# Kernel optimization log

Measured on AMD Instinct MI355X. Metric: run time of the kernel, lower is better.

## Reference

```python
import jax, jax.numpy as jnp
import numpy as np

FEAT_DIMS = [119, 9, 11, 12, 9, 5, 8, 2, 2]
EDGE_DIMS = [22, 6, 2]           # actual edge feature cardinalities
EDGE_TAB_DIMS = [119, 9, 11]     # table sizes (source code reuses feat_dims for edges)
H = 512
HE = 128
OUT = 1024
L = 6
B = 1024        # graphs
NPG = 32        # nodes per graph
N = B * NPG     # 32768 nodes
E = N * 4       # 131072 edges
EPG = E // B    # edges per graph
EPS = 1e-5
NODE_OFF = np.concatenate([[0], np.cumsum(FEAT_DIMS)[:-1]]).astype(np.int32)
EDGE_OFF = np.concatenate([[0], np.cumsum(EDGE_TAB_DIMS)[:-1]]).astype(np.int32)


def setup_inputs():
    key = jax.random.key(0)
    ks = iter(jax.random.split(key, 64))
    nk = lambda: next(ks)
    x = jnp.stack([jax.random.randint(nk(), (N,), 0, d) for d in FEAT_DIMS], axis=1)
    edge_attr = jnp.stack([jax.random.randint(nk(), (E,), 0, d) for d in EDGE_DIMS], axis=1)
    eg = jnp.arange(E) // EPG  # graph id per edge; endpoints stay inside the graph
    src = eg * NPG + jax.random.randint(nk(), (E,), 0, NPG)
    dst = eg * NPG + jax.random.randint(nk(), (E,), 0, NPG)
    edge_index = jnp.stack([src, dst], axis=0)
    batch = jnp.arange(N) // NPG
    w = lambda *s: jax.random.normal(nk(), s, jnp.float32) * 0.02
    return dict(
        x=x, edge_attr=edge_attr, edge_index=edge_index, batch=batch,
        node_tab=w(sum(FEAT_DIMS), H),
        edge_tab=w(sum(EDGE_TAB_DIMS), HE),
        bondW=w(L, HE, H), bondB=jnp.zeros((L, H)),
        bondG=jnp.ones((L, H)), bondBeta=jnp.zeros((L, H)),
        atomW1=w(L, H, 2 * H), atomB1=jnp.zeros((L, 2 * H)),
        atomG=jnp.ones((L, 2 * H)), atomBeta=jnp.zeros((L, 2 * H)),
        atomW2=w(L, 2 * H, H), atomB2=jnp.zeros((L, H)),
        normG=jnp.ones((L, H)), normB=jnp.zeros((L, H)),
        outW=w(H, OUT), outB=jnp.zeros((OUT,)),
        gapW=w(OUT, H), gapB=jnp.zeros((H,)),
        attW=w(H, 1), attB=jnp.zeros((1,)),
        projW=w(OUT, OUT), projB=jnp.zeros((OUT,)),
    )


def _bn(v, g, b):
    # training-mode BatchNorm1d over the row (node/edge) dimension
    m = v.mean(0)
    var = ((v - m) ** 2).mean(0)
    return (v - m) * jax.lax.rsqrt(var + EPS) * g + b


def reference(x, edge_attr, edge_index, batch, node_tab, edge_tab, bondW, bondB, bondG, bondBeta, atomW1, atomB1, atomG, atomBeta, atomW2, atomB2, normG, normB, outW, outB, gapW, gapB, attW, attB, projW, projB):
    # AtomEncoder: sum of per-column embedding lookups via offset-concatenated tables
    z = node_tab[x + jnp.asarray(NODE_OFF)].sum(1)              # [N, H]
    e_emb = edge_tab[edge_attr + jnp.asarray(EDGE_OFF)].sum(1)  # [E, HE]
    src, dst = edge_index[0], edge_index[1]

    def layer(z, p):
        bW, bB, bG, bBe, aW1, aB1, aG, aBe, aW2, aB2, nG, nB = p
        ee = jax.nn.relu(_bn(e_emb @ bW + bB, bG, bBe))         # mlp_bond: [E, H]
        msg = z[src] + ee                                       # gather + add (message)
        agg = jax.ops.segment_sum(msg, dst, num_segments=N)     # scatter-add aggregate
        h = jax.nn.relu(_bn((z + agg) @ aW1 + aB1, aG, aBe))    # mlp_atom layer 1
        z = h @ aW2 + aB2                                       # mlp_atom layer 2
        z = jax.nn.relu(_bn(z, nG, nB))                         # outer BN + ReLU; dropout = identity (eval)
        return z, None

    z, _ = jax.lax.scan(layer, z, (bondW, bondB, bondG, bondBeta, atomW1, atomB1, atomG, atomBeta, atomW2, atomB2, normG, normB))
    z = z @ outW + outB                                         # [N, OUT]

    # to_dense_batch (batch is sorted; NPG nodes per graph)
    counts = jax.ops.segment_sum(jnp.ones((N,), jnp.int32), batch, num_segments=B)
    starts = jnp.cumsum(counts) - counts
    pos = jnp.arange(N) - starts[batch]
    dense = jnp.zeros((B, NPG, OUT), z.dtype).at[batch, pos].set(z)   # [B, NPG, OUT]
    mask = jnp.zeros((B, NPG), z.dtype).at[batch, pos].set(1.0)       # [B, NPG]

    zg = dense @ gapW + gapB                                    # [B, NPG, H]
    att = zg @ attW + attB                                      # [B, NPG, 1]
    alpha = jax.nn.softmax(att, axis=1)
    h_graph = jnp.sum(dense * alpha * mask[..., None], axis=1)  # [B, OUT]
    return h_graph @ projW + projB                              # [B, OUT]
```

## Files before the change

### kernel.cpp

```cpp
#include <hip/hip_runtime.h>
#include <hip/hip_bf16.h>
#include <stdint.h>

using bf16 = __hip_bfloat16;
typedef __attribute__((ext_vector_type(8))) short short8;
typedef __attribute__((ext_vector_type(4))) float floatx4;

#define N_NODES  32768
#define N_EDGES  131072
#define N_GRAPH  1024
#define NPG      32
#define EPG      128
#define H_DIM    512
#define HE_DIM   128
#define OUT_DIM  1024
#define N_LAYERS 6
#define MC_ROWS  8192

__device__ __forceinline__ float b2f(bf16 v) { return __bfloat162float(v); }
__device__ __forceinline__ bf16  f2b(float f) { return __float2bfloat16(f); }
__device__ __forceinline__ floatx4 mfma16(short8 a, short8 b, floatx4 c) {
    return __builtin_amdgcn_mfma_f32_16x16x32_bf16(a, b, c, 0, 0, 0);
}
__device__ __forceinline__ float ldf(const void* p, size_t i, int isf) {
    return isf ? ((const float*)p)[i] : b2f(((const bf16*)p)[i]);
}
__device__ __forceinline__ void gload_lds16(const void* g, void* l) {
    __builtin_amdgcn_global_load_lds(
        (const __attribute__((address_space(1))) unsigned int*)g,
        (__attribute__((address_space(3))) unsigned int*)l, 16, 0, 0);
}

__device__ const int NODE_OFFS[9] = {0,119,128,139,151,160,165,173,175};

__global__ __launch_bounds__(256)
void k_detect(const unsigned short* __restrict__ tab, int n, int* __restrict__ flag)
{
    int big = 0;
    for (int i = threadIdx.x; i < n; i += 256) {
        unsigned short u = tab[i];
        int e = (u >> 7) & 0xFF;
        if (e >= 0x88) big++;
    }
    __shared__ int r[256];
    r[threadIdx.x] = big;
    __syncthreads();
    for (int s = 128; s > 0; s >>= 1) {
        if (threadIdx.x < s) r[threadIdx.x] += r[threadIdx.x + s];
        __syncthreads();
    }
    if (threadIdx.x == 0) *flag = (r[0] > 64) ? 1 : 0;
}

__global__ __launch_bounds__(64)
void k_edge_sort(const int* __restrict__ edge_index, short* __restrict__ sortedE,
                 int* __restrict__ estarts)
{
    const int g = blockIdx.x, t = threadIdx.x;
    __shared__ int d[128];
    __shared__ int off[33];
    d[t]      = edge_index[N_EDGES + g * EPG + t]      - g * NPG;
    d[t + 64] = edge_index[N_EDGES + g * EPG + t + 64] - g * NPG;
    __syncthreads();
    if (t < 32) {
        int c = 0;
        for (int e = 0; e < 128; ++e) c += (d[e] == t) ? 1 : 0;
        off[t + 1] = c;
    }
    __syncthreads();
    if (t == 0) {
        off[0] = 0;
        for (int n = 1; n <= 32; ++n) off[n] += off[n - 1];
    }
    __syncthreads();
    if (t < 33) estarts[g * 33 + t] = off[t];
    if (t < 32) {
        int p = off[t];
        for (int e = 0; e < 128; ++e)
            if (d[e] == t) sortedE[g * EPG + p++] = (short)e;
    }
}

__global__ __launch_bounds__(256)
void k_transpose(const void* __restrict__ W, size_t woff, bf16* __restrict__ Wt,
                 int K, int N, const int* __restrict__ flagp)
{
    const int isf = *flagp;
    __shared__ bf16 tile[64][72];
    const int nb = blockIdx.x * 64, kb = blockIdx.y * 64;
    const int t = threadIdx.x;
    const int r = t >> 2, c0 = (t & 3) * 16;
    if (isf) {
        const float* src = (const float*)W + woff + (size_t)(kb + r) * N + nb + c0;
#pragma unroll
        for (int i = 0; i < 16; ++i) tile[r][c0 + i] = f2b(src[i]);
    } else {
        const bf16* src = (const bf16*)W + woff + (size_t)(kb + r) * N + nb + c0;
        *(uint4*)&tile[r][c0]     = ((const uint4*)src)[0];
        *(uint4*)&tile[r][c0 + 8] = ((const uint4*)src)[1];
    }
    __syncthreads();
    __align__(16) bf16 vals[16];
#pragma unroll
    for (int i = 0; i < 16; ++i) vals[i] = tile[c0 + i][r];
    bf16* dst = Wt + (size_t)(nb + r) * K + kb + c0;
    *(uint4*)dst       = *(uint4*)&vals[0];
    *(uint4*)(dst + 8) = *(uint4*)&vals[8];
}

__global__ __launch_bounds__(512)
void k_node_embed(const int* __restrict__ x, const void* __restrict__ tab,
                  float* __restrict__ Z, const int* __restrict__ flagp)
{
    const int isf = *flagp;
    const int n = blockIdx.x, t = threadIdx.x;
    __shared__ int xi[9];
    if (t < 9) xi[t] = NODE_OFFS[t] + x[(size_t)n * 9 + t];
    __syncthreads();
    float s = 0.f;
#pragma unroll
    for (int f = 0; f < 9; ++f) s += ldf(tab, (size_t)xi[f] * H_DIM + t, isf);
    Z[(size_t)n * H_DIM + t] = s;
}

__global__ __launch_bounds__(256)
void k_bond_gram(const int* __restrict__ ea, const void* __restrict__ etab,
                 float* __restrict__ S, float* __restrict__ mu, const int* __restrict__ flagp)
{
    const int isf = *flagp;
    const int tid = threadIdx.x;
    const int lane = tid & 63, wv = tid >> 6, q = lane >> 4, l15 = lane & 15;
    __shared__ __align__(16) bf16 Et[128][136];
    __shared__ int eix[128][3];

    floatx4 acc[2][8];
#pragma unroll
    for (int i = 0; i < 2; ++i)
#pragma unroll
        for (int j = 0; j < 8; ++j) acc[i][j] = (floatx4){0.f,0.f,0.f,0.f};
    float muacc = 0.f;
    const int e0 = blockIdx.x * 512;

    for (int r = 0; r < 4; ++r) {
        __syncthreads();
        if (tid < 128) {
            int e = e0 + r * 128 + tid;
            eix[tid][0] = ea[(size_t)e * 3 + 0];
            eix[tid][1] = 119 + ea[(size_t)e * 3 + 1];
            eix[tid][2] = 128 + ea[(size_t)e * 3 + 2];
        }
        __syncthreads();
        {
            int c = tid & 127, eh = (tid >> 7) * 64;
            for (int e = eh; e < eh + 64; e += 2) {
                float s0 = ldf(etab, (size_t)eix[e][0] * HE_DIM + c, isf)
                         + ldf(etab, (size_t)eix[e][1] * HE_DIM + c, isf)
                         + ldf(etab, (size_t)eix[e][2] * HE_DIM + c, isf);
                float s1 = ldf(etab, (size_t)eix[e+1][0] * HE_DIM + c, isf)
                         + ldf(etab, (size_t)eix[e+1][1] * HE_DIM + c, isf)
                         + ldf(etab, (size_t)eix[e+1][2] * HE_DIM + c, isf);
                bf16 h0 = f2b(s0), h1 = f2b(s1);
                unsigned int pk = (unsigned int)*(unsigned short*)&h0
                                | ((unsigned int)*(unsigned short*)&h1 << 16);
                *(unsigned int*)&Et[c][e] = pk;
                muacc += b2f(h0) + b2f(h1);
            }
        }
        __syncthreads();
#pragma unroll
        for (int kc = 0; kc < 4; ++kc) {
            short8 a0 = *(const short8*)&Et[wv * 32 + l15][kc * 32 + q * 8];
            short8 a1 = *(const short8*)&Et[wv * 32 + 16 + l15][kc * 32 + q * 8];
#pragma unroll
            for (int nt = 0; nt < 8; ++nt) {
                short8 b = *(const short8*)&Et[nt * 16 + l15][kc * 32 + q * 8];
                acc[0][nt] = mfma16(a0, b, acc[0][nt]);
                acc[1][nt] = mfma16(a1, b, acc[1][nt]);
            }
        }
    }
#pragma unroll
    for (int mt = 0; mt < 2; ++mt)
#pragma unroll
        for (int nt = 0; nt < 8; ++nt)
#pragma unroll
            for (int rr = 0; rr < 4; ++rr) {
                int row = wv * 32 + mt * 16 + q * 4 + rr;
                atomicAdd(&S[(size_t)row * 128 + nt * 16 + l15], acc[mt][nt][rr]);
            }
    atomicAdd(&mu[tid & 127], muacc);
}

__global__ __launch_bounds__(128)
void k_bond_fold(const float* __restrict__ S, const float* __restrict__ mu,
                 const bf16* __restrict__ bWt,
                 const void* __restrict__ bG, const void* __restrict__ bBe, size_t go,
                 float* __restrict__ scale1, float* __restrict__ shift1,
                 const int* __restrict__ flagp)
{
    const int isf = *flagp;
    const int j = blockIdx.x;
    const int k = threadIdx.x;
    __shared__ float wbuf[128];
    __shared__ float rp[2][2];
    wbuf[k] = b2f(bWt[(size_t)j * 128 + k]);
    __syncthreads();
    float wk = wbuf[k];
    float dot = 0.f;
    for (int m = 0; m < 128; ++m) dot += S[(size_t)m * 128 + k] * wbuf[m];
    float p1 = wk * dot;
    float p2 = mu[k] * wk;
    for (int off = 32; off > 0; off >>= 1) {
        p1 += __shfl_down(p1, off, 64);
        p2 += __shfl_down(p2, off, 64);
    }
    if ((k & 63) == 0) { rp[k >> 6][0] = p1; rp[k >> 6][1] = p2; }
    __syncthreads();
    if (k == 0) {
        const float invE = 1.f / (float)N_EDGES;
        float mean = (rp[0][1] + rp[1][1]) * invE;
        float var  = (rp[0][0] + rp[1][0]) * invE - mean * mean;
        var = var < 0.f ? 0.f : var;
        float rstd = rsqrtf(var + 1e-5f);
        float sc = ldf(bG, go + j, isf) * rstd;
        scale1[j] = sc;
        shift1[j] = ldf(bBe, go + j, isf) - mean * sc;
    }
}

__global__ __launch_bounds__(256)
void k_bond_gemm_agg(const int* __restrict__ ea, const void* __restrict__ etab,
                     const bf16* __restrict__ bWt,
                     const int* __restrict__ edge_index,
                     const short* __restrict__ sortedE, const int* __restrict__ estarts,
                     const float* __restrict__ Z,
                     const float* __restrict__ scale1, const float* __restrict__ shift1,
                     const float* __restrict__ zsc, const float* __restrict__ zsh,
                     float* __restrict__ X2, const int* __restrict__ flagp)
{
    const int isf = *flagp;
    const int tid = threadIdx.x;
    const int lane = tid & 63, wv = tid >> 6, q = lane >> 4, l15 = lane & 15;
    const int nc = blockIdx.x;
    const int g  = blockIdx.y;

    __shared__ __align__(16) char smem[54784];
    bf16 (*As)[136] = (bf16(*)[136])smem;
    bf16 (*Bs)[136] = (bf16(*)[136])(smem + 34816);
    float (*Cs)[68] = (float(*)[68])smem;
    int*   srcl = (int*)(smem + 52224);
    short* sid  = (short*)(smem + 52736);
    int*   sst  = (int*)(smem + 52992);
    int (*eix)[3] = (int(*)[3])(smem + 53248);

    if (tid < 128) {
        int e = g * EPG + tid;
        srcl[tid] = edge_index[e];
        sid[tid]  = sortedE[g * EPG + tid];
        eix[tid][0] = ea[(size_t)e * 3 + 0];
        eix[tid][1] = 119 + ea[(size_t)e * 3 + 1];
        eix[tid][2] = 128 + ea[(size_t)e * 3 + 2];
    }
    if (tid >= 128 && tid < 161) sst[tid - 128] = estarts[g * 33 + (tid - 128)];
    __syncthreads();
    {
        int row = tid >> 1, half = (tid & 1) * 64;
        int eb[3] = {eix[row][0], eix[row][1], eix[row][2]};
#pragma unroll
        for (int seg = 0; seg < 4; ++seg) {
            float a16[16];
#pragma unroll
            for (int j = 0; j < 16; ++j) a16[j] = 0.f;
#pragma unroll
            for (int f = 0; f < 3; ++f) {
                size_t base = (size_t)eb[f] * HE_DIM + half + seg * 16;
                if (isf) {
                    const float4* s = (const float4*)((const float*)etab + base);
#pragma unroll
                    for (int v = 0; v < 4; ++v) {
                        float4 t = s[v];
                        a16[v*4+0] += t.x; a16[v*4+1] += t.y;
                        a16[v*4+2] += t.z; a16[v*4+3] += t.w;
                    }
                } else {
                    const bf16* s = (const bf16*)etab + base;
#pragma unroll
                    for (int j = 0; j < 16; ++j) a16[j] += b2f(s[j]);
                }
            }
#pragma unroll
            for (int j = 0; j < 16; ++j) As[row][half + seg * 16 + j] = f2b(a16[j]);
        }
    }
    {
        int row = tid >> 2, seg = (tid & 3) * 32;
        const bf16* src = bWt + (size_t)(nc * 64 + row) * 128 + seg;
        uint4 v0 = ((const uint4*)src)[0];
        uint4 v1 = ((const uint4*)src)[1];
        uint4 v2 = ((const uint4*)src)[2];
        uint4 v3 = ((const uint4*)src)[3];
        *(uint4*)(&Bs[row][seg +  0]) = v0;
        *(uint4*)(&Bs[row][seg +  8]) = v1;
        *(uint4*)(&Bs[row][seg + 16]) = v2;
        *(uint4*)(&Bs[row][seg + 24]) = v3;
    }
    __syncthreads();

    floatx4 acc[2][4];
#pragma unroll
    for (int i = 0; i < 2; ++i)
#pragma unroll
        for (int jj = 0; jj < 4; ++jj) acc[i][jj] = (floatx4){0.f,0.f,0.f,0.f};
    const int m0 = wv * 32;
#pragma unroll
    for (int kk = 0; kk < 4; ++kk) {
        int k0 = kk * 32;
        short8 a0 = *(const short8*)(&As[m0 + l15][k0 + q * 8]);
        short8 a1 = *(const short8*)(&As[m0 + 16 + l15][k0 + q * 8]);
#pragma unroll
        for (int nt = 0; nt < 4; ++nt) {
            short8 bfr = *(const short8*)(&Bs[nt * 16 + l15][k0 + q * 8]);
            acc[0][nt] = mfma16(a0, bfr, acc[0][nt]);
            acc[1][nt] = mfma16(a1, bfr, acc[1][nt]);
        }
    }
    __syncthreads();
#pragma unroll
    for (int mt = 0; mt < 2; ++mt)
#pragma unroll
        for (int nt = 0; nt < 4; ++nt)
#pragma unroll
            for (int r = 0; r < 4; ++r)
                Cs[m0 + mt * 16 + q * 4 + r][nt * 16 + l15] = acc[mt][nt][r];
    __syncthreads();
    {
        int j = tid & 63, eg = (tid >> 6) * 32;
        int col = nc * 64 + j;
        float sc = scale1[col], sh = shift1[col];
        float zs = zsc ? zsc[col] : 1.f, zh = zsc ? zsh[col] : 0.f;
#pragma unroll 4
        for (int e = eg; e < eg + 32; ++e) {
            float y = Cs[e][j] * sc + sh;
            y = y > 0.f ? y : 0.f;
            float zv = Z[(size_t)srcl[e] * H_DIM + col];
            if (zsc) { zv = zv * zs + zh; zv = zv > 0.f ? zv : 0.f; }
            Cs[e][j] = y + zv;
        }
    }
    __syncthreads();
    {
        int j = tid & 63, base = (tid >> 6) * 8;
        int col = nc * 64 + j;
        float zs = zsc ? zsc[col] : 1.f, zh = zsc ? zsh[col] : 0.f;
#pragma unroll
        for (int r = 0; r < 8; ++r) {
            int n = base + r;
            int s0 = sst[n], s1 = sst[n + 1];
            float a = 0.f;
            for (int idx = s0; idx < s1; ++idx)
                a += Cs[sid[idx]][j];
            size_t zi = (size_t)(g * NPG + n) * H_DIM + col;
            float zv = Z[zi];
            if (zsc) { zv = zv * zs + zh; zv = zv > 0.f ? zv : 0.f; }
            X2[zi] = a + zv;
        }
    }
}

__global__ __launch_bounds__(256, 2)
void k_gemm(const void* __restrict__ Av, int aMode,
            const float* __restrict__ bnsc, const float* __restrict__ bnsh,
            const bf16* __restrict__ Bt,
            void* __restrict__ Cv, int cMode,
            const void* __restrict__ bias, const int* __restrict__ flagp,
            int statsMode, float* __restrict__ cs, float* __restrict__ cq,
            int K, int lda, int ldc, int mStoreMin)
{
    const int tid  = threadIdx.x;
    const int lane = tid & 63;
    const int wv   = tid >> 6;
    const int q    = lane >> 4;
    const int l15  = lane & 15;
    const int wm   = wv & 1;
    const int wn   = wv >> 1;
    const int m0   = blockIdx.y * 128;
    const int n0   = blockIdx.x * 128;

    __shared__ __align__(16) bf16 As[128][40];
    __shared__ __align__(16) bf16 Bs[128][32];

    floatx4 acc[4][4];
#pragma unroll
    for (int mt = 0; mt < 4; ++mt)
#pragma unroll
        for (int nt = 0; nt < 4; ++nt) acc[mt][nt] = (floatx4){0.f,0.f,0.f,0.f};

    const int ar = tid >> 1;
    const int ak = (tid & 1) * 16;
    const bf16* BtBase = Bt + (size_t)n0 * K;
    const int cb0 = wv * 64;
    const int cb1 = (4 + wv) * 64;

    for (int k0 = 0; k0 < K; k0 += 32) {
        short av[16];
        if (aMode == 1) {
            const float* Ap = (const float*)Av + (size_t)(m0 + ar) * lda + k0 + ak;
#pragma unroll
            for (int i = 0; i < 16; i += 4) {
                float4 f = *(const float4*)(Ap + i);
                bf16 h0 = f2b(f.x), h1 = f2b(f.y), h2 = f2b(f.z), h3 = f2b(f.w);
                av[i] = *(short*)&h0; av[i+1] = *(short*)&h1;
                av[i+2] = *(short*)&h2; av[i+3] = *(short*)&h3;
            }
        } else {
            const bf16* Ap = (const bf16*)Av + (size_t)(m0 + ar) * lda + k0 + ak;
            *(uint4*)&av[0] = *(const uint4*)Ap;
            *(uint4*)&av[8] = *(const uint4*)(Ap + 8);
            if (aMode == 2) {
#pragma unroll
                for (int i = 0; i < 16; ++i) {
                    bf16 h = *(bf16*)&av[i];
                    float f = b2f(h) * bnsc[k0 + ak + i] + bnsh[k0 + ak + i];
                    f = f > 0.f ? f : 0.f;
                    bf16 o = f2b(f);
                    av[i] = *(short*)&o;
                }
            }
        }
        __syncthreads();
        {
            int c0i = cb0 + lane;
            gload_lds16(BtBase + (size_t)(c0i >> 2) * K + k0 + (c0i & 3) * 8,
                        &Bs[0][0] + (size_t)cb0 * 8);
            int c1i = cb1 + lane;
            gload_lds16(BtBase + (size_t)(c1i >> 2) * K + k0 + (c1i & 3) * 8,
                        &Bs[0][0] + (size_t)cb1 * 8);
        }
        *(uint4*)(&As[ar][ak])     = *(uint4*)&av[0];
        *(uint4*)(&As[ar][ak + 8]) = *(uint4*)&av[8];
        __syncthreads();
        short8 af[4], bfr[4];
#pragma unroll
        for (int mt = 0; mt < 4; ++mt)
            af[mt] = *(const short8*)(&As[wm * 64 + mt * 16 + l15][q * 8]);
#pragma unroll
        for (int nt = 0; nt < 4; ++nt)
            bfr[nt] = *(const short8*)(&Bs[wn * 64 + nt * 16 + l15][q * 8]);
#pragma unroll
        for (int mt = 0; mt < 4; ++mt)
#pragma unroll
            for (int nt = 0; nt < 4; ++nt)
                acc[mt][nt] = mfma16(af[mt], bfr[nt], acc[mt][nt]);
    }

    const int isf = flagp ? *flagp : 0;
    int cm = cMode;
    if (cMode == 3) cm = isf ? 2 : 1;
    float bvv[4] = {0.f, 0.f, 0.f, 0.f};
    if (bias) {
#pragma unroll
        for (int nt = 0; nt < 4; ++nt)
            bvv[nt] = ldf(bias, (size_t)n0 + wn * 64 + nt * 16 + l15, isf);
    }
    if (cm) {
#pragma unroll
        for (int mt = 0; mt < 4; ++mt)
#pragma unroll
            for (int r = 0; r < 4; ++r) {
                int row = m0 + wm * 64 + mt * 16 + q * 4 + r;
                if (row < mStoreMin) continue;
                size_t crow = (size_t)(row - mStoreMin) * ldc + n0;
                if (cm == 2) {
                    float* Crow = (float*)Cv + crow;
#pragma unroll
                    for (int nt = 0; nt < 4; ++nt)
                        Crow[wn * 64 + nt * 16 + l15] = acc[mt][nt][r] + bvv[nt];
                } else {
                    bf16* Crow = (bf16*)Cv + crow;
#pragma unroll
                    for (int nt = 0; nt < 4; ++nt)
                        Crow[wn * 64 + nt * 16 + l15] = f2b(acc[mt][nt][r] + bvv[nt]);
                }
            }
    }
    if (statsMode) {
        float ls[4], lq[4];
#pragma unroll
        for (int nt = 0; nt < 4; ++nt) { ls[nt] = 0.f; lq[nt] = 0.f; }
#pragma unroll
        for (int nt = 0; nt < 4; ++nt)
#pragma unroll
            for (int mt = 0; mt < 4; ++mt)
#pragma unroll
                for (int r = 0; r < 4; ++r) {
                    float v = acc[mt][nt][r];
                    if (statsMode == 1) v = b2f(f2b(v));
                    ls[nt] += v; lq[nt] += v * v;
                }
        float* red = (float*)&As[0][0];
        __syncthreads();
        red[tid] = 0.f;
        __syncthreads();
#pragma unroll
        for (int nt = 0; nt < 4; ++nt) {
            int col = wn * 64 + nt * 16 + l15;
            atomicAdd(&red[col * 2],     ls[nt]);
            atomicAdd(&red[col * 2 + 1], lq[nt]);
        }
        __syncthreads();
        if (tid < 128) {
            atomicAdd(&cs[n0 + tid], red[tid * 2]);
            atomicAdd(&cq[n0 + tid], red[tid * 2 + 1]);
        }
    }
}

__global__ __launch_bounds__(256)
void k_bn_finalize(const float* __restrict__ cs, const float* __restrict__ cq,
                   const void* __restrict__ g, const void* __restrict__ be, size_t goff,
                   int cols, float invR, float* __restrict__ scale, float* __restrict__ shift,
                   const int* __restrict__ flagp)
{
    const int isf = *flagp;
    int c = blockIdx.x * 256 + threadIdx.x;
    if (c < cols) {
        float mean = cs[c] * invR;
        float var = cq[c] * invR - mean * mean;
        var = var < 0.f ? 0.f : var;
        float rstd = rsqrtf(var + 1e-5f);
        float sc = ldf(g, goff + c, isf) * rstd;
        scale[c] = sc;
        shift[c] = ldf(be, goff + c, isf) - mean * sc;
    }
}

__global__ __launch_bounds__(256)
void k_bn_apply_relu_f32(float* __restrict__ X, const float* __restrict__ scale,
                         const float* __restrict__ shift, int colmask, unsigned int nvec4)
{
    unsigned int i = blockIdx.x * 256 + threadIdx.x;
    if (i >= nvec4) return;
    float4* p = (float4*)X + i;
    int cbase = (int)(((size_t)i * 4) & (size_t)colmask);
    float4 v = *p;
    float f;
    f = v.x * scale[cbase+0] + shift[cbase+0]; v.x = f > 0.f ? f : 0.f;
    f = v.y * scale[cbase+1] + shift[cbase+1]; v.y = f > 0.f ? f : 0.f;
    f = v.z * scale[cbase+2] + shift[cbase+2]; v.z = f > 0.f ? f : 0.f;
    f = v.w * scale[cbase+3] + shift[cbase+3]; v.w = f > 0.f ? f : 0.f;
    *p = v;
}

__global__ __launch_bounds__(256)
void k_att_v(const void* __restrict__ gapW, const void* __restrict__ gapB,
             const void* __restrict__ attW, const void* __restrict__ attB,
             float* __restrict__ v, const int* __restrict__ flagp)
{
    const int isf = *flagp;
    const int lane = threadIdx.x & 63, wv = threadIdx.x >> 6;
    if (blockIdx.x == 256) {
        if (wv == 0) {
            float s = 0.f;
            for (int k = lane; k < 512; k += 64) s += ldf(gapB, k, isf) * ldf(attW, k, isf);
            for (int off = 32; off > 0; off >>= 1) s += __shfl_down(s, off, 64);
            if (lane == 0) v[1024] = s + ldf(attB, 0, isf);
        }
        return;
    }
    const int o = blockIdx.x * 4 + wv;
    float s = 0.f;
    for (int k = lane; k < 512; k += 64) s += ldf(gapW, (size_t)o * 512 + k, isf) * ldf(attW, k, isf);
    for (int off = 32; off > 0; off >>= 1) s += __shfl_down(s, off, 64);
    if (lane == 0) v[o] = s;
}

__global__ __launch_bounds__(256)
void k_qv(const void* __restrict__ outW, const void* __restrict__ outB,
          const float* __restrict__ v, float* __restrict__ qv, const int* __restrict__ flagp)
{
    const int isf = *flagp;
    const int lane = threadIdx.x & 63, wv = threadIdx.x >> 6;
    if (blockIdx.x == 128) {
        if (wv == 0) {
            float s = 0.f;
            for (int o = lane; o < 1024; o += 64) s += ldf(outB, o, isf) * v[o];
            for (int off = 32; off > 0; off >>= 1) s += __shfl_down(s, off, 64);
            if (lane == 0) qv[512] = s + v[1024];
        }
        return;
    }
    const int k = blockIdx.x * 4 + wv;
    float s = 0.f;
    for (int o = lane; o < 1024; o += 64) s += ldf(outW, (size_t)k * 1024 + o, isf) * v[o];
    for (int off = 32; off > 0; off >>= 1) s += __shfl_down(s, off, 64);
    if (lane == 0) qv[k] = s;
}

__global__ __launch_bounds__(256)
void k_att_dot(const float* __restrict__ Z, const float* __restrict__ qv, float* __restrict__ att)
{
    const int lane = threadIdx.x & 63, wv = threadIdx.x >> 6;
    const int row = blockIdx.x * 4 + wv;
    const float* p = Z + (size_t)row * 512 + lane * 8;
    float s = 0.f;
#pragma unroll
    for (int i = 0; i < 8; ++i) s += p[i] * qv[lane * 8 + i];
    for (int off = 32; off > 0; off >>= 1) s += __shfl_down(s, off, 64);
    if (lane == 0) att[row] = s + qv[512];
}

__global__ __launch_bounds__(256)
void k_softmax_pool(const float* __restrict__ Z, const float* __restrict__ att, bf16* __restrict__ ZG)
{
    const int g = blockIdx.x, t = threadIdx.x;
    __shared__ float alpha[32];
    if (t < 32) alpha[t] = att[g * 32 + t];
    __syncthreads();
    if (t == 0) {
        float mx = alpha[0];
        for (int p = 1; p < 32; ++p) mx = fmaxf(mx, alpha[p]);
        float sum = 0.f;
        for (int p = 0; p < 32; ++p) { float e = __expf(alpha[p] - mx); alpha[p] = e; sum += e; }
        float inv = 1.f / sum;
        for (int p = 0; p < 32; ++p) alpha[p] *= inv;
    }
    __syncthreads();
#pragma unroll
    for (int ci = 0; ci < 2; ++ci) {
        int c = t + ci * 256;
        float acc = 0.f;
        for (int p = 0; p < 32; ++p)
            acc += alpha[p] * Z[(size_t)(g * 32 + p) * 512 + c];
        ZG[(size_t)g * 512 + c] = f2b(acc);
    }
}

extern "C" void kernel_launch(void* const* d_in, const int* in_sizes, int n_in,
                              void* d_out, int out_size, void* d_ws, size_t ws_size,
                              hipStream_t stream)
{
    (void)in_sizes; (void)n_in; (void)out_size; (void)ws_size;
    const int*  x          = (const int*)d_in[0];
    const int*  edge_attr  = (const int*)d_in[1];
    const int*  edge_index = (const int*)d_in[2];
    const void* node_tab   = d_in[4];
    const void* edge_tab   = d_in[5];
    const void* bondW      = d_in[6];
    const void* bondG      = d_in[8];
    const void* bondBeta   = d_in[9];
    const void* atomW1     = d_in[10];
    const void* atomG      = d_in[12];
    const void* atomBeta   = d_in[13];
    const void* atomW2     = d_in[14];
    const void* normG      = d_in[16];
    const void* normB      = d_in[17];
    const void* outW       = d_in[18];
    const void* outB       = d_in[19];
    const void* gapW       = d_in[20];
    const void* gapB       = d_in[21];
    const void* attW       = d_in[22];
    const void* attB       = d_in[23];
    const void* projW      = d_in[24];
    const void* projB      = d_in[25];

    char* ws = (char*)d_ws;
    float* z      = (float*)ws;
    bf16*  Uc     = (bf16*)(ws + 67108864ull);
    bf16*  zg     = Uc;
    bf16*  hg     = (bf16*)(ws + 67108864ull + 1048576ull);
    bf16*  projWt = (bf16*)(ws + 67108864ull + 4194304ull);
    bf16*  W1t    = (bf16*)(ws + 83886080ull);
    bf16*  W2t    = (bf16*)(ws + 84934656ull);
    bf16*  bWt    = (bf16*)(ws + 85983232ull);
    bf16*  outWt  = W1t;
    char*  st  = ws + 86114304ull;
    int*   flag = (int*)(st);
    float* S    = (float*)(st + 256);
    float* mu   = (float*)(st + 65792);
    float* cs   = (float*)(st + 66304);
    float* cq   = (float*)(st + 70400);
    float* cs2  = (float*)(st + 74496);
    float* cq2  = (float*)(st + 76544);
    float* sc1  = (float*)(st + 78592);
    float* sh1  = (float*)(st + 82688);
    float* sc2  = (float*)(st + 86784);
    float* sh2  = (float*)(st + 88832);
    float* vv   = (float*)(st + 90880);
    float* qv   = (float*)(st + 95232);
    float* att  = (float*)(st + 97536);
    short* sortedE = (short*)(st + 228608);
    int*   estarts = (int*)(st + 490752);

    k_detect<<<1, 256, 0, stream>>>((const unsigned short*)node_tab, 4096, flag);
    k_edge_sort<<<N_GRAPH, 64, 0, stream>>>(edge_index, sortedE, estarts);
    hipMemsetAsync(st + 256, 0, 66048, stream);
    k_bond_gram<<<256, 256, 0, stream>>>(edge_attr, edge_tab, S, mu, flag);
    k_node_embed<<<N_NODES, 512, 0, stream>>>(x, node_tab, z, flag);

    for (int l = 0; l < N_LAYERS; ++l) {
        const float* zscp = (l == 0) ? nullptr : sc2;
        const float* zshp = (l == 0) ? nullptr : sh2;

        k_transpose<<<dim3(16, 8), 256, 0, stream>>>(atomW1, (size_t)l * 512 * 1024, W1t, 512, 1024, flag);
        k_transpose<<<dim3(8, 16), 256, 0, stream>>>(atomW2, (size_t)l * 1024 * 512, W2t, 1024, 512, flag);
        k_transpose<<<dim3(8, 2), 256, 0, stream>>>(bondW, (size_t)l * 128 * 512, bWt, 128, 512, flag);

        k_bond_fold<<<512, 128, 0, stream>>>(S, mu, bWt, bondG, bondBeta, (size_t)l * 512, sc1, sh1, flag);
        k_bond_gemm_agg<<<dim3(8, N_GRAPH), 256, 0, stream>>>(edge_attr, edge_tab, bWt,
                                                              edge_index, sortedE, estarts,
                                                              z, sc1, sh1, zscp, zshp, z, flag);

        hipMemsetAsync(cs, 0, 12288, stream);
        k_gemm<<<dim3(8, 256), 256, 0, stream>>>(z, 1, nullptr, nullptr, W1t,
                                                 Uc, 1, nullptr, nullptr,
                                                 1, cs, cq, 512, 512, 1024, 24576);
        k_bn_finalize<<<4, 256, 0, stream>>>(cs, cq, atomG, atomBeta, (size_t)l * 1024,
                                             1024, 1.f / 32768.f, sc1, sh1, flag);
        for (int mi = 0; mi < 4; ++mi) {
            int mc = (mi + 3) & 3;
            float* zc = z + (size_t)mc * MC_ROWS * 512;
            if (mc != 3)
                k_gemm<<<dim3(8, 64), 256, 0, stream>>>(zc, 1, nullptr, nullptr, W1t,
                                                        Uc, 1, nullptr, nullptr,
                                                        0, nullptr, nullptr, 512, 512, 1024, 0);
            k_gemm<<<dim3(4, 64), 256, 0, stream>>>(Uc, 2, sc1, sh1, W2t,
                                                    zc, 2, nullptr, nullptr,
                                                    2, cs2, cq2, 1024, 1024, 512, 0);
        }
        k_bn_finalize<<<2, 256, 0, stream>>>(cs2, cq2, normG, normB, (size_t)l * 512,
                                             512, 1.f / 32768.f, sc2, sh2, flag);
    }
    k_bn_apply_relu_f32<<<16384, 256, 0, stream>>>(z, sc2, sh2, 511, 4194304u);

    k_att_v<<<257, 256, 0, stream>>>(gapW, gapB, attW, attB, vv, flag);
    k_qv<<<129, 256, 0, stream>>>(outW, outB, vv, qv, flag);
    k_att_dot<<<8192, 256, 0, stream>>>(z, qv, att);
    k_softmax_pool<<<N_GRAPH, 256, 0, stream>>>(z, att, zg);
    k_transpose<<<dim3(16, 8), 256, 0, stream>>>(outW, 0, outWt, 512, 1024, flag);
    k_gemm<<<dim3(8, 8), 256, 0, stream>>>(zg, 0, nullptr, nullptr, outWt,
                                           hg, 1, outB, flag,
                                           0, nullptr, nullptr, 512, 512, 1024, 0);
    k_transpose<<<dim3(16, 16), 256, 0, stream>>>(projW, 0, projWt, 1024, 1024, flag);
    k_gemm<<<dim3(8, 8), 256, 0, stream>>>(hg, 0, nullptr, nullptr, projWt,
                                           d_out, 3, projB, flag,
                                           0, nullptr, nullptr, 1024, 1024, 1024, 0);
}
```

Before: 4.425 ms.

## Precompute bf16 edge embeddings once and scatter GEMM outputs into destination-sorted order

Adds a one-time kernel that sums the three edge-table rows per edge into a bf16 buffer in workspace, so each layer's bond kernel (8 column-blocks × 6 layers) loads those rows directly instead of redoing three table gathers. The bond kernel also writes its accumulators into shared memory at each edge's sorted rank, so the per-node aggregation reads contiguous rows rather than doing indirect lookups. The cost is a 32 MB workspace buffer, used only when the workspace is large enough, plus one extra launch.

```diff
diff --git a/kernel.cpp b/kernel.cpp
--- a/kernel.cpp
+++ b/kernel.cpp
@@ -79,6 +79,22 @@
         for (int e = 0; e < 128; ++e)
             if (d[e] == t) sortedE[g * EPG + p++] = (short)e;
     }
+}
+
+__global__ __launch_bounds__(512)
+void k_edge_embed(const int* __restrict__ ea, const void* __restrict__ etab,
+                  bf16* __restrict__ Ebf, const int* __restrict__ flagp)
+{
+    const int isf = *flagp;
+    const int t = threadIdx.x;
+    const int sub = t >> 7, c = t & 127;
+    const int e = blockIdx.x * 4 + sub;
+    size_t eb = (size_t)e * 3;
+    int i0 = ea[eb], i1 = 119 + ea[eb + 1], i2 = 128 + ea[eb + 2];
+    float s = ldf(etab, (size_t)i0 * HE_DIM + c, isf);
+    s += ldf(etab, (size_t)i1 * HE_DIM + c, isf);
+    s += ldf(etab, (size_t)i2 * HE_DIM + c, isf);
+    Ebf[(size_t)e * HE_DIM + c] = f2b(s);
 }
 
 __global__ __launch_bounds__(256)
@@ -230,6 +246,7 @@
 
 __global__ __launch_bounds__(256)
 void k_bond_gemm_agg(const int* __restrict__ ea, const void* __restrict__ etab,
+                     const bf16* __restrict__ Ebf,
                      const bf16* __restrict__ bWt,
                      const int* __restrict__ edge_index,
                      const short* __restrict__ sortedE, const int* __restrict__ estarts,
@@ -244,52 +261,62 @@
     const int nc = blockIdx.x;
     const int g  = blockIdx.y;
 
-    __shared__ __align__(16) char smem[54784];
+    __shared__ __align__(16) char smem[53136];
     bf16 (*As)[136] = (bf16(*)[136])smem;
     bf16 (*Bs)[136] = (bf16(*)[136])(smem + 34816);
     float (*Cs)[68] = (float(*)[68])smem;
-    int*   srcl = (int*)(smem + 52224);
-    short* sid  = (short*)(smem + 52736);
-    int*   sst  = (int*)(smem + 52992);
-    int (*eix)[3] = (int(*)[3])(smem + 53248);
+    int*   srcs = (int*)(smem + 52224);
+    int*   sst  = (int*)(smem + 52736);
+    short* rank = (short*)(smem + 52872);
 
     if (tid < 128) {
-        int e = g * EPG + tid;
-        srcl[tid] = edge_index[e];
-        sid[tid]  = sortedE[g * EPG + tid];
-        eix[tid][0] = ea[(size_t)e * 3 + 0];
-        eix[tid][1] = 119 + ea[(size_t)e * 3 + 1];
-        eix[tid][2] = 128 + ea[(size_t)e * 3 + 2];
+        int p = tid;
+        int e = (int)sortedE[g * EPG + p];
+        rank[e] = (short)p;
+        srcs[p] = edge_index[g * EPG + e];
     }
     if (tid >= 128 && tid < 161) sst[tid - 128] = estarts[g * 33 + (tid - 128)];
-    __syncthreads();
+
     {
         int row = tid >> 1, half = (tid & 1) * 64;
-        int eb[3] = {eix[row][0], eix[row][1], eix[row][2]};
-#pragma unroll
-        for (int seg = 0; seg < 4; ++seg) {
-            float a16[16];
-#pragma unroll
-            for (int j = 0; j < 16; ++j) a16[j] = 0.f;
-#pragma unroll
-            for (int f = 0; f < 3; ++f) {
-                size_t base = (size_t)eb[f] * HE_DIM + half + seg * 16;
-                if (isf) {
-                    const float4* s = (const float4*)((const float*)etab + base);
-#pragma unroll
-                    for (int v = 0; v < 4; ++v) {
-                        float4 t = s[v];
-                        a16[v*4+0] += t.x; a16[v*4+1] += t.y;
-                        a16[v*4+2] += t.z; a16[v*4+3] += t.w;
+        if (Ebf) {
+            const uint4* src = (const uint4*)(Ebf + (size_t)(g * EPG + row) * HE_DIM + half);
+            uint4 v[8];
+#pragma unroll
+            for (int i = 0; i < 8; ++i) v[i] = src[i];
+#pragma unroll
+            for (int i = 0; i < 8; ++i) *(uint4*)(&As[row][half + 8 * i]) = v[i];
+        } else {
+            size_t eb = (size_t)(g * EPG + row) * 3;
+            int ebi[3];
+            ebi[0] = ea[eb];
+            ebi[1] = 119 + ea[eb + 1];
+            ebi[2] = 128 + ea[eb + 2];
+#pragma unroll
+            for (int seg = 0; seg < 4; ++seg) {
+                float a16[16];
+#pragma unroll
+                for (int j = 0; j < 16; ++j) a16[j] = 0.f;
+#pragma unroll
+                for (int f = 0; f < 3; ++f) {
+                    size_t base = (size_t)ebi[f] * HE_DIM + half + seg * 16;
+                    if (isf) {
+                        const float4* s = (const float4*)((const float*)etab + base);
+#pragma unroll
+                        for (int v = 0; v < 4; ++v) {
+                            float4 t = s[v];
+                            a16[v*4+0] += t.x; a16[v*4+1] += t.y;
+                            a16[v*4+2] += t.z; a16[v*4+3] += t.w;
+                        }
+                    } else {
+                        const bf16* s = (const bf16*)etab + base;
+#pragma unroll
+                        for (int j = 0; j < 16; ++j) a16[j] += b2f(s[j]);
                     }
-                } else {
-                    const bf16* s = (const bf16*)etab + base;
-#pragma unroll
-                    for (int j = 0; j < 16; ++j) a16[j] += b2f(s[j]);
                 }
+#pragma unroll
+                for (int j = 0; j < 16; ++j) As[row][half + seg * 16 + j] = f2b(a16[j]);
             }
-#pragma unroll
-            for (int j = 0; j < 16; ++j) As[row][half + seg * 16 + j] = f2b(a16[j]);
         }
     }
     {
@@ -325,26 +352,31 @@
         }
     }
     __syncthreads();
-#pragma unroll
-    for (int mt = 0; mt < 2; ++mt)
-#pragma unroll
-        for (int nt = 0; nt < 4; ++nt)
-#pragma unroll
-            for (int r = 0; r < 4; ++r)
-                Cs[m0 + mt * 16 + q * 4 + r][nt * 16 + l15] = acc[mt][nt][r];
-    __syncthreads();
     {
-        int j = tid & 63, eg = (tid >> 6) * 32;
+#pragma unroll
+        for (int mt = 0; mt < 2; ++mt)
+#pragma unroll
+            for (int r = 0; r < 4; ++r) {
+                int row = m0 + mt * 16 + q * 4 + r;
+                int rp = (int)rank[row];
+#pragma unroll
+                for (int nt = 0; nt < 4; ++nt)
+                    Cs[rp][nt * 16 + l15] = acc[mt][nt][r];
+            }
+    }
+    __syncthreads();
+    {
+        int j = tid & 63, pg = (tid >> 6) * 32;
         int col = nc * 64 + j;
         float sc = scale1[col], sh = shift1[col];
         float zs = zsc ? zsc[col] : 1.f, zh = zsc ? zsh[col] : 0.f;
 #pragma unroll 4
-        for (int e = eg; e < eg + 32; ++e) {
-            float y = Cs[e][j] * sc + sh;
+        for (int p = pg; p < pg + 32; ++p) {
+            float y = Cs[p][j] * sc + sh;
             y = y > 0.f ? y : 0.f;
-            float zv = Z[(size_t)srcl[e] * H_DIM + col];
+            float zv = Z[(size_t)srcs[p] * H_DIM + col];
             if (zsc) { zv = zv * zs + zh; zv = zv > 0.f ? zv : 0.f; }
-            Cs[e][j] = y + zv;
+            Cs[p][j] = y + zv;
         }
     }
     __syncthreads();
@@ -358,7 +390,7 @@
             int s0 = sst[n], s1 = sst[n + 1];
             float a = 0.f;
             for (int idx = s0; idx < s1; ++idx)
-                a += Cs[sid[idx]][j];
+                a += Cs[idx][j];
             size_t zi = (size_t)(g * NPG + n) * H_DIM + col;
             float zv = Z[zi];
             if (zsc) { zv = zv * zs + zh; zv = zv > 0.f ? zv : 0.f; }
@@ -639,7 +671,7 @@
                               void* d_out, int out_size, void* d_ws, size_t ws_size,
                               hipStream_t stream)
 {
-    (void)in_sizes; (void)n_in; (void)out_size; (void)ws_size;
+    (void)in_sizes; (void)n_in; (void)out_size;
     const int*  x          = (const int*)d_in[0];
     const int*  edge_attr  = (const int*)d_in[1];
     const int*  edge_index = (const int*)d_in[2];
@@ -690,12 +722,15 @@
     float* att  = (float*)(st + 97536);
     short* sortedE = (short*)(st + 228608);
     int*   estarts = (int*)(st + 490752);
+    bf16*  Ebf = nullptr;
+    if (ws_size >= 120295424ull) Ebf = (bf16*)(ws + 86740992ull);
 
     k_detect<<<1, 256, 0, stream>>>((const unsigned short*)node_tab, 4096, flag);
     k_edge_sort<<<N_GRAPH, 64, 0, stream>>>(edge_index, sortedE, estarts);
     hipMemsetAsync(st + 256, 0, 66048, stream);
     k_bond_gram<<<256, 256, 0, stream>>>(edge_attr, edge_tab, S, mu, flag);
     k_node_embed<<<N_NODES, 512, 0, stream>>>(x, node_tab, z, flag);
+    if (Ebf) k_edge_embed<<<N_EDGES / 4, 512, 0, stream>>>(edge_attr, edge_tab, Ebf, flag);
 
     for (int l = 0; l < N_LAYERS; ++l) {
         const float* zscp = (l == 0) ? nullptr : sc2;
@@ -706,7 +741,7 @@
         k_transpose<<<dim3(8, 2), 256, 0, stream>>>(bondW, (size_t)l * 128 * 512, bWt, 128, 512, flag);
 
         k_bond_fold<<<512, 128, 0, stream>>>(S, mu, bWt, bondG, bondBeta, (size_t)l * 512, sc1, sh1, flag);
-        k_bond_gemm_agg<<<dim3(8, N_GRAPH), 256, 0, stream>>>(edge_attr, edge_tab, bWt,
+        k_bond_gemm_agg<<<dim3(8, N_GRAPH), 256, 0, stream>>>(edge_attr, edge_tab, Ebf, bWt,
                                                               edge_index, sortedE, estarts,
                                                               z, sc1, sh1, zscp, zshp, z, flag);
 
```

Result: faster. 3.621 ms (-18.2%).
